# Kernel tuning notes

Measured on AMD Instinct MI355X. Metric: run time of the kernel, lower is better.

Reference implementation:

```python
import jax, jax.numpy as jnp
import numpy as np

S, HID, H, D, G = 2048, 4096, 32, 128, 2   # seq, hidden, heads, head_dim, kv groups
ROT = D // 2                               # rotary applied to first half of head_dim
QKV = HID + 2 * G * D                      # 4608


def setup_inputs() -> dict:
    key = jax.random.key(0)
    k1, k2, k3 = jax.random.split(key, 3)
    sc = 0.02
    return {
        "hidden_states": jax.random.normal(k1, (S, HID), jnp.float32),
        "W_qkv": jax.random.normal(k2, (HID, QKV), jnp.float32) * sc,
        "b_qkv": jnp.zeros((QKV,), jnp.float32),
        "W_dense": jax.random.normal(k3, (HID, HID), jnp.float32) * sc,
    }


def _rope(x, pos):
    # x: [S, n_heads, ROT]; interleaved-pair rotation (ChatGLM2 convention)
    half = ROT // 2
    inv_freq = 10000.0 ** (-jnp.arange(0, ROT, 2, dtype=jnp.float32) / ROT)  # [half]
    theta = pos[:, None] * inv_freq                                          # [S, half]
    cos = jnp.cos(theta)[:, None, :]
    sin = jnp.sin(theta)[:, None, :]
    xp = x.reshape(x.shape[0], x.shape[1], half, 2)
    x0, x1 = xp[..., 0], xp[..., 1]
    out = jnp.stack([x0 * cos - x1 * sin, x1 * cos + x0 * sin], axis=-1)
    return out.reshape(x.shape)


def reference(hidden_states, W_qkv, b_qkv, W_dense):
    qkv = hidden_states @ W_qkv + b_qkv            # [S, QKV]
    q = qkv[:, : H * D].reshape(S, H, D)           # [S, H, D]
    k = qkv[:, H * D : H * D + G * D].reshape(S, G, D)
    v = qkv[:, H * D + G * D :].reshape(S, G, D)

    pos = jnp.arange(S, dtype=jnp.float32)
    q = jnp.concatenate([_rope(q[..., :ROT], pos), q[..., ROT:]], axis=-1)
    k = jnp.concatenate([_rope(k[..., :ROT], pos), k[..., ROT:]], axis=-1)

    gidx = jnp.arange(H) % G                       # head -> kv group (MQA/GQA)
    kh = k[:, gidx, :]                             # [S, H, D]
    vh = v[:, gidx, :]

    scores = jnp.einsum('shd,thd->hst', q, kh) / jnp.sqrt(jnp.float32(D))
    causal = jnp.tril(jnp.ones((S, S), bool))
    scores = jnp.where(causal[None], scores, jnp.float32(-1e9))
    p = jax.nn.softmax(scores, axis=-1)            # [H, S, S]
    ctx = jnp.einsum('hst,thd->shd', p, vh).reshape(S, HID)
    return ctx @ W_dense
```

## Files before the change

### kernel.cpp

```cpp
#include <hip/hip_runtime.h>
#include <hip/hip_bf16.h>

#define S_LEN 2048
#define HIDN  4096
#define NH    32
#define HD    128
#define QKV_N 4608
#define K_OFF 4096
#define V_OFF 4352
#define SCALE 0.08838834764831845f

typedef __attribute__((ext_vector_type(8))) short   short8;
typedef __attribute__((ext_vector_type(4))) float   f32x4;
typedef __attribute__((ext_vector_type(16))) float  f32x16;
typedef __attribute__((ext_vector_type(4))) unsigned short ushort4v;
typedef __attribute__((ext_vector_type(8))) unsigned short ushort8;

typedef __attribute__((address_space(1))) const unsigned int GU32;
typedef __attribute__((address_space(3))) unsigned int LU32;

__device__ __forceinline__ void async16(const void* g, void* l) {
  __builtin_amdgcn_global_load_lds((GU32*)g, (LU32*)l, 16, 0, 0);
}

__device__ __forceinline__ unsigned short f2bf(float x) {
  __hip_bfloat16 h = __float2bfloat16(x);
  return *reinterpret_cast<unsigned short*>(&h);
}
__device__ __forceinline__ float bf2f(unsigned short u) {
  __hip_bfloat16 h = *reinterpret_cast<__hip_bfloat16*>(&u);
  return __bfloat162float(h);
}

__global__ void k_cvt_bf16(const float* __restrict__ in, unsigned short* __restrict__ out, int n4) {
  int i = blockIdx.x * 256 + threadIdx.x;
  if (i >= n4) return;
  const float4 v = reinterpret_cast<const float4*>(in)[i];
  ushort4v o = { f2bf(v.x), f2bf(v.y), f2bf(v.z), f2bf(v.w) };
  reinterpret_cast<ushort4v*>(out)[i] = o;
}

__global__ __launch_bounds__(256) void k_transpose_cvt(const float* __restrict__ W,
                                                       unsigned short* __restrict__ WT,
                                                       int K, int N) {
  __shared__ float tl[64][65];
  const int n0 = blockIdx.x * 64, k0 = blockIdx.y * 64;
  const int t = threadIdx.x;
  const int r = t >> 4, c4 = (t & 15) << 2;
#pragma unroll
  for (int p = 0; p < 4; ++p) {
    int krow = p * 16 + r;
    const float4 v = *reinterpret_cast<const float4*>(&W[(size_t)(k0 + krow) * N + n0 + c4]);
    tl[krow][c4 + 0] = v.x; tl[krow][c4 + 1] = v.y;
    tl[krow][c4 + 2] = v.z; tl[krow][c4 + 3] = v.w;
  }
  __syncthreads();
#pragma unroll
  for (int p = 0; p < 4; ++p) {
    int nrow = p * 16 + r;
    ushort4v o = { f2bf(tl[c4 + 0][nrow]), f2bf(tl[c4 + 1][nrow]),
                   f2bf(tl[c4 + 2][nrow]), f2bf(tl[c4 + 3][nrow]) };
    *reinterpret_cast<ushort4v*>(&WT[(size_t)(n0 + nrow) * K + k0 + c4]) = o;
  }
}

template <int BIAS, int OUTBF>
__global__ __launch_bounds__(256, 2) void k_gemm_bt(const unsigned short* __restrict__ A,
                                                    const unsigned short* __restrict__ Bt,
                                                    const float* __restrict__ bias,
                                                    void* __restrict__ Cout,
                                                    int M, int N, int K) {
  __shared__ __align__(16) unsigned char lds[32768];
  const int tid = threadIdx.x;
  const int l = tid & 63, w = tid >> 6;
  const int wr = w >> 1, wc = w & 1;
  const int l16 = l & 15, lh = l >> 4;
  const int nx = N >> 7;
  const int cpx = gridDim.x >> 3;
  const int wg = (blockIdx.x & 7) * cpx + (blockIdx.x >> 3);
  const int m0 = (wg / nx) * 128, n0 = (wg % nx) * 128;
  const size_t rowK = (size_t)K * 2;
  const char* Ab = (const char*)A + (size_t)m0 * rowK;
  const char* Bb = (const char*)Bt + (size_t)n0 * rowK;
  f32x4 acc[4][4] = {};
  const int nkt = K >> 6;
  for (int kt = 0; kt < nkt; ++kt) {
    const int kbyte = kt << 7;
#pragma unroll
    for (int rr = 0; rr < 4; ++rr) {
      int off = rr * 4096 + tid * 16;
      int row = off >> 7;
      int col = (off & 127) ^ ((row & 7) << 4);
      async16(Ab + (size_t)row * rowK + kbyte + col, lds + off);
    }
#pragma unroll
    for (int rr = 0; rr < 4; ++rr) {
      int off = rr * 4096 + tid * 16;
      int row = off >> 7;
      int col = (off & 127) ^ ((row & 7) << 4);
      async16(Bb + (size_t)row * rowK + kbyte + col, lds + 16384 + off);
    }
    __syncthreads();
#pragma unroll
    for (int kk = 0; kk < 2; ++kk) {
      short8 af[4], bfr[4];
#pragma unroll
      for (int m = 0; m < 4; ++m) {
        int arow = wr * 64 + m * 16 + l16;
        int byte = (arow << 7) + kk * 64 + lh * 16;
        byte ^= (arow & 7) << 4;
        af[m] = *reinterpret_cast<const short8*>(lds + byte);
      }
#pragma unroll
      for (int n = 0; n < 4; ++n) {
        int brow = wc * 64 + n * 16 + l16;
        int byte = (brow << 7) + kk * 64 + lh * 16;
        byte ^= (brow & 7) << 4;
        bfr[n] = *reinterpret_cast<const short8*>(lds + 16384 + byte);
      }
#pragma unroll
      for (int m = 0; m < 4; ++m)
#pragma unroll
        for (int n = 0; n < 4; ++n)
          acc[m][n] = __builtin_amdgcn_mfma_f32_16x16x32_bf16(af[m], bfr[n], acc[m][n], 0, 0, 0);
    }
    __syncthreads();
  }
#pragma unroll
  for (int m = 0; m < 4; ++m) {
    int grow = m0 + wr * 64 + m * 16 + lh * 4;
#pragma unroll
    for (int n = 0; n < 4; ++n) {
      int gcol = n0 + wc * 64 + n * 16 + l16;
      float bv = BIAS ? bias[gcol] : 0.f;
      f32x4 v = acc[m][n];
#pragma unroll
      for (int j = 0; j < 4; ++j) {
        float val = v[j] + bv;
        if (OUTBF) ((unsigned short*)Cout)[(size_t)(grow + j) * N + gcol] = f2bf(val);
        else       ((float*)Cout)[(size_t)(grow + j) * N + gcol] = val;
      }
    }
  }
}

__global__ void k_rope(unsigned short* __restrict__ qkv) {
  const int p = blockIdx.x * 64 + threadIdx.x;
  const int s = blockIdx.y;
  const int i = p & 31;
  const int hh = p >> 5;
  const int col = (hh < 32) ? (hh * HD + 2 * i) : (K_OFF + (hh - 32) * HD + 2 * i);
  unsigned int* ptr = (unsigned int*)(qkv + (size_t)s * QKV_N + col);
  unsigned int both = *ptr;
  float x0 = bf2f((unsigned short)(both & 0xffffu));
  float x1 = bf2f((unsigned short)(both >> 16));
  float inv = expf(-0.28782313662425572f * (float)i);
  float theta = (float)s * inv;
  float sn, cs;
  sincosf(theta, &sn, &cs);
  float y0 = x0 * cs - x1 * sn;
  float y1 = x1 * cs + x0 * sn;
  *ptr = (unsigned int)f2bf(y0) | ((unsigned int)f2bf(y1) << 16);
}

__global__ __launch_bounds__(256) void k_transpose_v(const unsigned short* __restrict__ qkv,
                                                     unsigned short* __restrict__ Vt) {
  __shared__ __align__(16) unsigned short tl[64][72];
  const int st = blockIdx.x * 64;
  const int dt = blockIdx.y * 64;
  const int g = blockIdx.z;
  const int t = threadIdx.x;
  const int r = t >> 3;
  const int seg = (t & 7) * 8;
#pragma unroll
  for (int p = 0; p < 2; ++p) {
    int srow = p * 32 + r;
    ushort8 v = *reinterpret_cast<const ushort8*>(
        &qkv[(size_t)(st + srow) * QKV_N + V_OFF + g * HD + dt + seg]);
    *reinterpret_cast<ushort8*>(&tl[srow][seg]) = v;
  }
  __syncthreads();
#pragma unroll
  for (int p = 0; p < 2; ++p) {
    int drow = p * 32 + r;
    ushort8 o;
#pragma unroll
    for (int i = 0; i < 8; ++i) o[i] = tl[seg + i][drow];
    *reinterpret_cast<ushort8*>(&Vt[((size_t)g * HD + dt + drow) * S_LEN + st + seg]) = o;
  }
}

__device__ __forceinline__ void stage_kv2(const char* Kb, const char* Vb,
                                          unsigned char* ldsK, unsigned char* ldsV, int tid) {
  __builtin_amdgcn_sched_barrier(0);
#pragma unroll
  for (int rr = 0; rr < 4; ++rr) {
    int off = rr * 4096 + tid * 16;
    int row = off >> 8;
    int col = (off & 255) ^ ((row & 15) << 4);
    async16(Kb + (size_t)row * (QKV_N * 2) + col, ldsK + off);
  }
#pragma unroll
  for (int rr = 0; rr < 4; ++rr) {
    int off = rr * 4096 + tid * 16;
    int row = off >> 7;
    int col = (off & 127) ^ ((row & 7) << 4);
    async16(Vb + (size_t)row * (S_LEN * 2) + col, ldsV + off);
  }
  __builtin_amdgcn_sched_barrier(0);
}

__global__ __launch_bounds__(256) void k_attn(const unsigned short* __restrict__ qkv,
                                              const unsigned short* __restrict__ Vt,
                                              unsigned short* __restrict__ ctx) {
  __shared__ __align__(16) unsigned char lds[81920];
  const int tid = threadIdx.x;
  const int l = tid & 63, w = tid >> 6;
  const int l32 = l & 31, hi = l >> 5;
  const int b = blockIdx.x;
  const int h = b & 31;
  const int g = h & 1;
  const int bt = b >> 5;
  const int tier = (b < 256) ? bt : 23 - bt;
  const int q0 = (15 - tier) * 128;
  const int qw = q0 + w * 32;
  const int nkt = (q0 >> 6) + 2;

  const char* Kbase = (const char*)(qkv + K_OFF + g * HD);
  const char* Vbase = (const char*)(Vt + (size_t)g * HD * S_LEN);

  short8 vones;
#pragma unroll
  for (int e = 0; e < 8; ++e) vones[e] = (short)0x3F80;

  short8 qf[8];
#pragma unroll
  for (int ks = 0; ks < 8; ++ks)
    qf[ks] = *reinterpret_cast<const short8*>(
        qkv + (size_t)(qw + l32) * QKV_N + h * HD + ks * 16 + hi * 8);
  asm volatile("s_waitcnt vmcnt(0)" ::: "memory");

  f32x16 o[4] = {};
  f32x16 lacc = {};
  float m_run = -1e30f;

  stage_kv2(Kbase, Vbase, lds, lds + 32768, tid);

  for (int kt = 0; kt < nkt; ++kt) {
    const int k0 = kt << 6;
    if (kt + 1 < nkt) {
      const int bsel = ((kt + 1) & 1) * 16384;
      stage_kv2(Kbase + (size_t)(k0 + 64) * (QKV_N * 2), Vbase + (size_t)(k0 + 64) * 2,
                lds + bsel, lds + 32768 + bsel, tid);
      asm volatile("s_waitcnt vmcnt(8)" ::: "memory");
    } else {
      asm volatile("s_waitcnt vmcnt(0)" ::: "memory");
    }
    __builtin_amdgcn_s_barrier();
    __builtin_amdgcn_sched_barrier(0);

    const unsigned char* Kl = lds + (kt & 1) * 16384;
    const unsigned char* Vl = lds + 32768 + (kt & 1) * 16384;

    const bool active = (qw + 31 >= k0);
    if (active) {
      f32x16 sf[2] = {};
      __builtin_amdgcn_s_setprio(1);
#pragma unroll
      for (int ks = 0; ks < 8; ++ks)
#pragma unroll
        for (int kb = 0; kb < 2; ++kb) {
          int krow = kb * 32 + l32;
          int byte = krow * 256 + ks * 32 + hi * 16;
          byte ^= (krow & 15) << 4;
          short8 kf = *reinterpret_cast<const short8*>(Kl + byte);
          sf[kb] = __builtin_amdgcn_mfma_f32_32x32x16_bf16(qf[ks], kf, sf[kb], 0, 0, 0);
        }
      __builtin_amdgcn_s_setprio(0);

      float tmax = -1e30f;
#pragma unroll
      for (int kb = 0; kb < 2; ++kb) {
        int key = k0 + kb * 32 + l32;
#pragma unroll
        for (int r = 0; r < 16; ++r) {
          int qrow = qw + (r & 3) + 8 * (r >> 2) + 4 * hi;
          float v = sf[kb][r] * SCALE;
          v = (key <= qrow) ? v : -1e30f;
          sf[kb][r] = v;
          tmax = fmaxf(tmax, v);
        }
      }
#pragma unroll
      for (int d = 1; d < 64; d <<= 1) tmax = fmaxf(tmax, __shfl_xor(tmax, d, 64));
      if (tmax > m_run + 8.f) {
        float fsc = __expf(m_run - tmax);
        m_run = tmax;
#pragma unroll
        for (int nf = 0; nf < 4; ++nf) o[nf] *= fsc;
        lacc *= fsc;
      }

      unsigned char* Pw = lds + 65536 + w * 4096;
#pragma unroll
      for (int kb = 0; kb < 2; ++kb)
#pragma unroll
        for (int r = 0; r < 16; ++r) {
          int row = (r & 3) + 8 * (r >> 2) + 4 * hi;
          int byte = row * 128 + (kb * 32 + l32) * 2;
          byte ^= (row & 7) << 4;
          *(unsigned short*)(Pw + byte) = f2bf(__expf(sf[kb][r] - m_run));
        }

      __builtin_amdgcn_s_setprio(1);
#pragma unroll
      for (int ks4 = 0; ks4 < 4; ++ks4) {
        int pbyte = l32 * 128 + (ks4 * 16 + hi * 8) * 2;
        pbyte ^= (l32 & 7) << 4;
        short8 pa = *reinterpret_cast<const short8*>(Pw + pbyte);
        lacc = __builtin_amdgcn_mfma_f32_32x32x16_bf16(pa, vones, lacc, 0, 0, 0);
#pragma unroll
        for (int nf = 0; nf < 4; ++nf) {
          int drow = nf * 32 + l32;
          int vbyte = drow * 128 + ks4 * 32 + hi * 16;
          vbyte ^= (drow & 7) << 4;
          short8 vb = *reinterpret_cast<const short8*>(Vl + vbyte);
          o[nf] = __builtin_amdgcn_mfma_f32_32x32x16_bf16(pa, vb, o[nf], 0, 0, 0);
        }
      }
      __builtin_amdgcn_s_setprio(0);
    }
    __builtin_amdgcn_s_barrier();
  }

#pragma unroll
  for (int nf = 0; nf < 4; ++nf) {
    int col = h * HD + nf * 32 + l32;
#pragma unroll
    for (int r = 0; r < 16; ++r) {
      int row = qw + (r & 3) + 8 * (r >> 2) + 4 * hi;
      ctx[(size_t)row * HIDN + col] = f2bf(o[nf][r] / lacc[r]);
    }
  }
}

extern "C" void kernel_launch(void* const* d_in, const int* in_sizes, int n_in,
                              void* d_out, int out_size, void* d_ws, size_t ws_size,
                              hipStream_t stream) {
  const float* hidden = (const float*)d_in[0];
  const float* Wqkv = (const float*)d_in[1];
  const float* bqkv = (const float*)d_in[2];
  const float* Wd = (const float*)d_in[3];
  char* ws = (char*)d_ws;
  unsigned short* hid_bf = (unsigned short*)(ws);
  unsigned short* WqkvT  = (unsigned short*)(ws + 16777216);
  unsigned short* WdT    = (unsigned short*)(ws + 54525952);
  unsigned short* qkv    = (unsigned short*)(ws + 88080384);
  unsigned short* Vt     = (unsigned short*)(ws + 106954752);
  unsigned short* ctx    = (unsigned short*)(ws + 108003328);

  k_cvt_bf16<<<8192, 256, 0, stream>>>(hidden, hid_bf, 2097152);
  k_transpose_cvt<<<dim3(72, 64), 256, 0, stream>>>(Wqkv, WqkvT, 4096, 4608);
  k_transpose_cvt<<<dim3(64, 64), 256, 0, stream>>>(Wd, WdT, 4096, 4096);
  k_gemm_bt<1, 1><<<576, 256, 0, stream>>>(hid_bf, WqkvT, bqkv, qkv, 2048, 4608, 4096);
  k_rope<<<dim3(17, 2048), 64, 0, stream>>>(qkv);
  k_transpose_v<<<dim3(32, 2, 2), 256, 0, stream>>>(qkv, Vt);
  k_attn<<<512, 256, 0, stream>>>(qkv, Vt, ctx);
  k_gemm_bt<0, 0><<<512, 256, 0, stream>>>(ctx, WdT, nullptr, d_out, 2048, 4096, 4096);
}
```

Baseline: 344.6 us.

## Keep softmax probabilities in registers via transposed QK^T and permlane swaps

```diff
diff --git a/kernel.cpp b/kernel.cpp
--- a/kernel.cpp
+++ b/kernel.cpp
@@ -15,6 +15,7 @@
 typedef __attribute__((ext_vector_type(16))) float  f32x16;
 typedef __attribute__((ext_vector_type(4))) unsigned short ushort4v;
 typedef __attribute__((ext_vector_type(8))) unsigned short ushort8;
+typedef __attribute__((ext_vector_type(4))) unsigned int uint4v;
 
 typedef __attribute__((address_space(1))) const unsigned int GU32;
 typedef __attribute__((address_space(3))) unsigned int LU32;
@@ -213,7 +214,7 @@
 __global__ __launch_bounds__(256) void k_attn(const unsigned short* __restrict__ qkv,
                                               const unsigned short* __restrict__ Vt,
                                               unsigned short* __restrict__ ctx) {
-  __shared__ __align__(16) unsigned char lds[81920];
+  __shared__ __align__(16) unsigned char lds[65536];
   const int tid = threadIdx.x;
   const int l = tid & 63, w = tid >> 6;
   const int l32 = l & 31, hi = l >> 5;
@@ -274,23 +275,23 @@
           int byte = krow * 256 + ks * 32 + hi * 16;
           byte ^= (krow & 15) << 4;
           short8 kf = *reinterpret_cast<const short8*>(Kl + byte);
-          sf[kb] = __builtin_amdgcn_mfma_f32_32x32x16_bf16(qf[ks], kf, sf[kb], 0, 0, 0);
+          sf[kb] = __builtin_amdgcn_mfma_f32_32x32x16_bf16(kf, qf[ks], sf[kb], 0, 0, 0);
         }
       __builtin_amdgcn_s_setprio(0);
 
+      const int qrow = qw + l32;
+      f32x16 p[2];
       float tmax = -1e30f;
 #pragma unroll
-      for (int kb = 0; kb < 2; ++kb) {
-        int key = k0 + kb * 32 + l32;
+      for (int kb = 0; kb < 2; ++kb)
 #pragma unroll
         for (int r = 0; r < 16; ++r) {
-          int qrow = qw + (r & 3) + 8 * (r >> 2) + 4 * hi;
+          int key = k0 + kb * 32 + (r & 3) + 8 * (r >> 2) + 4 * hi;
           float v = sf[kb][r] * SCALE;
           v = (key <= qrow) ? v : -1e30f;
-          sf[kb][r] = v;
+          p[kb][r] = v;
           tmax = fmaxf(tmax, v);
         }
-      }
 #pragma unroll
       for (int d = 1; d < 64; d <<= 1) tmax = fmaxf(tmax, __shfl_xor(tmax, d, 64));
       if (tmax > m_run + 8.f) {
@@ -300,29 +301,42 @@
         for (int nf = 0; nf < 4; ++nf) o[nf] *= fsc;
         lacc *= fsc;
       }
-
-      unsigned char* Pw = lds + 65536 + w * 4096;
 #pragma unroll
       for (int kb = 0; kb < 2; ++kb)
 #pragma unroll
-        for (int r = 0; r < 16; ++r) {
-          int row = (r & 3) + 8 * (r >> 2) + 4 * hi;
-          int byte = row * 128 + (kb * 32 + l32) * 2;
-          byte ^= (row & 7) << 4;
-          *(unsigned short*)(Pw + byte) = f2bf(__expf(sf[kb][r] - m_run));
+        for (int r = 0; r < 16; ++r)
+          p[kb][r] = __expf(p[kb][r] - m_run);
+
+      unsigned int pk[2][8];
+#pragma unroll
+      for (int kb = 0; kb < 2; ++kb)
+#pragma unroll
+        for (int j = 0; j < 8; ++j) {
+          int r0 = 4 * (j >> 1) + 2 * (j & 1);
+          float lo = p[kb][r0], hiv = p[kb][r0 + 1];
+          asm("v_cvt_pk_bf16_f32 %0, %1, %2" : "=v"(pk[kb][j]) : "v"(lo), "v"(hiv));
         }
+#pragma unroll
+      for (int kb = 0; kb < 2; ++kb) {
+        asm volatile("v_permlane32_swap_b32 %0, %1" : "+v"(pk[kb][0]), "+v"(pk[kb][2]));
+        asm volatile("v_permlane32_swap_b32 %0, %1" : "+v"(pk[kb][1]), "+v"(pk[kb][3]));
+        asm volatile("v_permlane32_swap_b32 %0, %1" : "+v"(pk[kb][4]), "+v"(pk[kb][6]));
+        asm volatile("v_permlane32_swap_b32 %0, %1" : "+v"(pk[kb][5]), "+v"(pk[kb][7]));
+      }
 
       __builtin_amdgcn_s_setprio(1);
 #pragma unroll
-      for (int ks4 = 0; ks4 < 4; ++ks4) {
-        int pbyte = l32 * 128 + (ks4 * 16 + hi * 8) * 2;
-        pbyte ^= (l32 & 7) << 4;
-        short8 pa = *reinterpret_cast<const short8*>(Pw + pbyte);
+      for (int ks = 0; ks < 4; ++ks) {
+        const int kb = ks >> 1, half = ks & 1;
+        uint4v t;
+        t.x = pk[kb][half * 4 + 0]; t.y = pk[kb][half * 4 + 1];
+        t.z = pk[kb][half * 4 + 2]; t.w = pk[kb][half * 4 + 3];
+        short8 pa = __builtin_bit_cast(short8, t);
         lacc = __builtin_amdgcn_mfma_f32_32x32x16_bf16(pa, vones, lacc, 0, 0, 0);
 #pragma unroll
         for (int nf = 0; nf < 4; ++nf) {
           int drow = nf * 32 + l32;
-          int vbyte = drow * 128 + ks4 * 32 + hi * 16;
+          int vbyte = drow * 128 + ks * 32 + hi * 16;
           vbyte ^= (drow & 7) << 4;
           short8 vb = *reinterpret_cast<const short8*>(Vl + vbyte);
           o[nf] = __builtin_amdgcn_mfma_f32_32x32x16_bf16(pa, vb, o[nf], 0, 0, 0);
```

After: 334.7 us. 2.9% less time.
